# Kernel tuning notes

Measured on AMD Instinct MI355X. Metric: run time of the kernel, lower is better.

The kernel has to match this reference:

```python
import jax, jax.numpy as jnp
import numpy as np

D_MODEL = 512
NHEAD = 8
WINDOW = 64


def setup_inputs() -> dict:
    key = jax.random.key(0)
    ks = jax.random.split(key, 5)
    d = D_MODEL
    x = jax.random.normal(ks[0], (8, 2048, d), dtype=jnp.float32)
    # nn.MultiheadAttention params: packed in-proj [3d, d] + bias [3d], out-proj [d, d] + bias [d]
    scale = 1.0 / np.sqrt(d)
    in_proj_w = jax.random.normal(ks[1], (3 * d, d), dtype=jnp.float32) * scale
    in_proj_b = jnp.zeros((3 * d,), dtype=jnp.float32)
    out_proj_w = jax.random.normal(ks[2], (d, d), dtype=jnp.float32) * scale
    out_proj_b = jnp.zeros((d,), dtype=jnp.float32)
    return {"x": x, "in_proj_w": in_proj_w, "in_proj_b": in_proj_b,
            "out_proj_w": out_proj_w, "out_proj_b": out_proj_b}


def reference(x, in_proj_w, in_proj_b, out_proj_w, out_proj_b):
    B, L, d = x.shape
    H = NHEAD
    dh = d // H
    # packed qkv projection (torch Linear: x @ W.T + b)
    qkv = jnp.einsum('bld,ed->ble', x, in_proj_w) + in_proj_b  # [B, L, 3d]
    q, k, v = jnp.split(qkv, 3, axis=-1)
    # split heads -> [B, H, L, dh]
    def heads(t):
        return t.reshape(B, L, H, dh).transpose(0, 2, 1, 3)
    q, k, v = heads(q), heads(k), heads(v)
    scores = jnp.einsum('bhqd,bhkd->bhqk', q, k) / jnp.sqrt(jnp.float32(dh))
    # banded mask: positions with |i-j| > window are masked out
    idx = jnp.arange(L)
    band = jnp.abs(idx[None, :] - idx[:, None]) > WINDOW  # [L, L] bool
    scores = jnp.where(band[None, None, :, :], jnp.float32(-jnp.inf), scores)
    p = jax.nn.softmax(scores, axis=-1)
    out = jnp.einsum('bhqk,bhkd->bhqd', p, v)  # [B, H, L, dh]
    out = out.transpose(0, 2, 1, 3).reshape(B, L, d)
    return jnp.einsum('bld,ed->ble', out, out_proj_w) + out_proj_b
```

## Files before the change

kernel.cpp:

```cpp
#include <hip/hip_runtime.h>

typedef __bf16 bf16x8 __attribute__((ext_vector_type(8)));
typedef unsigned short u16;
typedef unsigned short u16x8 __attribute__((ext_vector_type(8)));
typedef float f32x4 __attribute__((ext_vector_type(4)));

#define L_SEQ 2048
#define NQT   (L_SEQ / 128)
#define SB()  __builtin_amdgcn_sched_barrier(0)

__device__ __forceinline__ float bf2f(u16 x) {
    unsigned u = ((unsigned)x) << 16;
    return __builtin_bit_cast(float, u);
}
__device__ __forceinline__ u16 f2bf(float f) {
    unsigned u = __builtin_bit_cast(unsigned, f);
    u += 0x7FFFu + ((u >> 16) & 1u);
    return (u16)(u >> 16);
}

__device__ __forceinline__ void gload_lds16(const u16* g, u16* l) {
    __builtin_amdgcn_global_load_lds(
        (const __attribute__((address_space(1))) void*)g,
        (__attribute__((address_space(3))) void*)l, 16, 0, 0);
}

__global__ void cvt_w(const float* __restrict__ wi, const float* __restrict__ wo,
                      u16* __restrict__ wio, u16* __restrict__ woo,
                      int nwi8, int nwo8) {
    int i = blockIdx.x * blockDim.x + threadIdx.x;
    const float* src; u16* dst;
    if (i < nwi8) { src = wi; dst = wio; }
    else if (i < nwi8 + nwo8) { i -= nwi8; src = wo; dst = woo; }
    else return;
    const float4* p = reinterpret_cast<const float4*>(src) + (size_t)i * 2;
    const float4 a = p[0], b = p[1];
    u16x8 r;
    r[0] = f2bf(a.x); r[1] = f2bf(a.y); r[2] = f2bf(a.z); r[3] = f2bf(a.w);
    r[4] = f2bf(b.x); r[5] = f2bf(b.y); r[6] = f2bf(b.z); r[7] = f2bf(b.w);
    *(reinterpret_cast<u16x8*>(dst) + i) = r;
}

__launch_bounds__(512, 4)
__global__ void gemm_qkv(const float* __restrict__ A, const u16* __restrict__ W,
                         const float* __restrict__ bias, u16* __restrict__ C,
                         int M, int N, int K) {
    __shared__ u16 As[3][256 * 32];
    __shared__ u16 Bs[3][128 * 32];

    const int tid   = threadIdx.x;
    const int lane  = tid & 63;
    const int wid   = tid >> 6;
    const int wm    = wid >> 1;
    const int wn    = wid & 1;
    const int row_l = lane & 15;
    const int grp   = lane >> 4;

    const int nwg  = gridDim.x * gridDim.y;
    const int hw   = blockIdx.y * gridDim.x + blockIdx.x;
    const int tile = (hw & 7) * (nwg >> 3) + (hw >> 3);
    const int m0 = (tile / gridDim.x) * 256;
    const int n0 = (tile % gridDim.x) * 128;

    const int arow = tid >> 1;
    const int av   = (arow >> 1) & 3;
    const int g0   = ((tid & 1) * 2)     ^ av;
    const int g1   = ((tid & 1) * 2 + 1) ^ av;
    const float* gA0 = A + (size_t)(m0 + arow) * K + g0 * 8;
    const float* gA1 = A + (size_t)(m0 + arow) * K + g1 * 8;

    const int brow = tid >> 2;
    const int bcol = ((tid & 3) ^ ((tid >> 3) & 3)) * 8;
    const u16* gB = W + (size_t)(n0 + brow) * K + bcol;

    f32x4 acc[4][4];
#pragma unroll
    for (int mi = 0; mi < 4; ++mi)
#pragma unroll
        for (int ni = 0; ni < 4; ++ni)
            acc[mi][ni] = (f32x4){0.f, 0.f, 0.f, 0.f};

    const int rchunk = (grp ^ ((row_l >> 1) & 3)) * 8;
    const int NT = K >> 5;

    {
        const f32x4* q0 = reinterpret_cast<const f32x4*>(gA0);
        const f32x4* q1 = reinterpret_cast<const f32x4*>(gA1);
        f32x4 p00 = q0[0], p01 = q0[1], p10 = q1[0], p11 = q1[1];
        SB();
        gload_lds16(gB,      &Bs[0][0] + wid * 512);
        SB();
        gload_lds16(gB + 32, &Bs[1][0] + wid * 512);
        SB();
        asm volatile("s_waitcnt vmcnt(2)" ::: "memory");
        SB();
        u16x8 w0, w1;
#pragma unroll
        for (int e = 0; e < 4; ++e) {
            w0[e] = f2bf(p00[e]); w0[4 + e] = f2bf(p01[e]);
            w1[e] = f2bf(p10[e]); w1[4 + e] = f2bf(p11[e]);
        }
        *reinterpret_cast<u16x8*>(&As[0][(2 * tid + 0) * 8]) = w0;
        *reinterpret_cast<u16x8*>(&As[0][(2 * tid + 1) * 8]) = w1;
        asm volatile("s_waitcnt vmcnt(1)" ::: "memory");
        asm volatile("s_waitcnt lgkmcnt(0)" ::: "memory");
        __builtin_amdgcn_s_barrier();
    }

    int buf = 0;
    for (int t = 0; t < NT; ++t) {
        bf16x8 a[4], b[4];
#pragma unroll
        for (int mi = 0; mi < 4; ++mi)
            a[mi] = *reinterpret_cast<const bf16x8*>(
                &As[buf][(wm * 64 + mi * 16 + row_l) * 32 + rchunk]);
#pragma unroll
        for (int ni = 0; ni < 4; ++ni)
            b[ni] = *reinterpret_cast<const bf16x8*>(
                &Bs[buf][(wn * 64 + ni * 16 + row_l) * 32 + rchunk]);
        SB();
        f32x4 p00, p01, p10, p11;
        if (t + 1 < NT) {
            const f32x4* q0 = reinterpret_cast<const f32x4*>(gA0 + (t + 1) * 32);
            const f32x4* q1 = reinterpret_cast<const f32x4*>(gA1 + (t + 1) * 32);
            p00 = q0[0]; p01 = q0[1]; p10 = q1[0]; p11 = q1[1];
        }
        SB();
        if (t + 2 < NT) {
            int sb = buf + 2; if (sb >= 3) sb -= 3;
            gload_lds16(gB + (size_t)(t + 2) * 32, &Bs[sb][0] + wid * 512);
        }
        SB();
        asm volatile("s_waitcnt lgkmcnt(0)" ::: "memory");
        SB();
        __builtin_amdgcn_s_setprio(1);
#pragma unroll
        for (int mi = 0; mi < 4; ++mi)
#pragma unroll
            for (int ni = 0; ni < 4; ++ni)
                acc[mi][ni] = __builtin_amdgcn_mfma_f32_16x16x32_bf16(a[mi], b[ni], acc[mi][ni], 0, 0, 0);
        __builtin_amdgcn_s_setprio(0);
        SB();
        if (t + 1 < NT) {
            if (t + 2 < NT) asm volatile("s_waitcnt vmcnt(1)" ::: "memory");
            else            asm volatile("s_waitcnt vmcnt(0)" ::: "memory");
            SB();
            int wb = buf + 1; if (wb >= 3) wb -= 3;
            u16x8 w0, w1;
#pragma unroll
            for (int e = 0; e < 4; ++e) {
                w0[e] = f2bf(p00[e]); w0[4 + e] = f2bf(p01[e]);
                w1[e] = f2bf(p10[e]); w1[4 + e] = f2bf(p11[e]);
            }
            *reinterpret_cast<u16x8*>(&As[wb][(2 * tid + 0) * 8]) = w0;
            *reinterpret_cast<u16x8*>(&As[wb][(2 * tid + 1) * 8]) = w1;
            asm volatile("s_waitcnt lgkmcnt(0)" ::: "memory");
            __builtin_amdgcn_s_barrier();
        }
        buf = buf + 1; if (buf >= 3) buf = 0;
    }

#pragma unroll
    for (int ni = 0; ni < 4; ++ni) {
        const int col = n0 + wn * 64 + ni * 16 + row_l;
        const float bsf = bias[col];
#pragma unroll
        for (int mi = 0; mi < 4; ++mi) {
#pragma unroll
            for (int r = 0; r < 4; ++r) {
                const int rowm = m0 + wm * 64 + mi * 16 + grp * 4 + r;
                C[(size_t)rowm * N + col] = f2bf(acc[mi][ni][r] + bsf);
            }
        }
    }
}

template <bool OUT_BF16>
__launch_bounds__(256, 3)
__global__ void gemm_ring(const u16* __restrict__ A, const u16* __restrict__ W,
                          const float* __restrict__ bias, void* __restrict__ Cv,
                          int M, int N, int K) {
    __shared__ u16 As[3][128 * 32];
    __shared__ u16 Bs[3][128 * 32];

    const int tid   = threadIdx.x;
    const int lane  = tid & 63;
    const int wid   = tid >> 6;
    const int wm    = wid >> 1;
    const int wn    = wid & 1;
    const int row_l = lane & 15;
    const int grp   = lane >> 4;

    const int nwg  = gridDim.x * gridDim.y;
    const int hw   = blockIdx.y * gridDim.x + blockIdx.x;
    const int tile = (hw & 7) * (nwg >> 3) + (hw >> 3);
    const int m0 = (tile / gridDim.x) * 128;
    const int n0 = (tile % gridDim.x) * 128;

    const int srow = tid >> 2;
    const int scol = ((tid & 3) ^ ((tid >> 3) & 3)) * 8;
    const u16* gA = A + (size_t)(m0 + srow) * K + scol;
    const u16* gB = W + (size_t)(n0 + srow) * K + scol;

    f32x4 acc[4][4];
#pragma unroll
    for (int mi = 0; mi < 4; ++mi)
#pragma unroll
        for (int ni = 0; ni < 4; ++ni)
            acc[mi][ni] = (f32x4){0.f, 0.f, 0.f, 0.f};

    auto stage = [&](int buf, int kt) {
#pragma unroll
        for (int i = 0; i < 2; ++i) {
            gload_lds16(gA + (size_t)(i * 64) * K + kt * 32, &As[buf][i * 2048 + wid * 512]);
            gload_lds16(gB + (size_t)(i * 64) * K + kt * 32, &Bs[buf][i * 2048 + wid * 512]);
        }
    };

    const int rchunk = (grp ^ ((row_l >> 1) & 3)) * 8;

    auto compute = [&](int buf) {
        bf16x8 a[4], b[4];
#pragma unroll
        for (int mi = 0; mi < 4; ++mi)
            a[mi] = *reinterpret_cast<const bf16x8*>(
                &As[buf][(wm * 64 + mi * 16 + row_l) * 32 + rchunk]);
#pragma unroll
        for (int ni = 0; ni < 4; ++ni)
            b[ni] = *reinterpret_cast<const bf16x8*>(
                &Bs[buf][(wn * 64 + ni * 16 + row_l) * 32 + rchunk]);
        __builtin_amdgcn_s_setprio(1);
#pragma unroll
        for (int mi = 0; mi < 4; ++mi)
#pragma unroll
            for (int ni = 0; ni < 4; ++ni)
                acc[mi][ni] = __builtin_amdgcn_mfma_f32_16x16x32_bf16(a[mi], b[ni], acc[mi][ni], 0, 0, 0);
        __builtin_amdgcn_s_setprio(0);
    };

    const int NT = K >> 5;
    stage(0, 0);
    stage(1, 1);
    int cur = 0;
    for (int t = 0; t < NT; ++t) {
        if (t == NT - 1) asm volatile("s_waitcnt vmcnt(0)" ::: "memory");
        else             asm volatile("s_waitcnt vmcnt(4)" ::: "memory");
        __builtin_amdgcn_s_barrier();
        if (t + 2 < NT) {
            int st = cur + 2; if (st >= 3) st -= 3;
            stage(st, t + 2);
        }
        compute(cur);
        cur = cur + 1; if (cur >= 3) cur = 0;
    }

#pragma unroll
    for (int ni = 0; ni < 4; ++ni) {
        const int col = n0 + wn * 64 + ni * 16 + row_l;
        const float bsf = bias[col];
#pragma unroll
        for (int mi = 0; mi < 4; ++mi) {
#pragma unroll
            for (int r = 0; r < 4; ++r) {
                const int rowm = m0 + wm * 64 + mi * 16 + grp * 4 + r;
                const float v = acc[mi][ni][r] + bsf;
                if (OUT_BF16)
                    ((u16*)Cv)[(size_t)rowm * N + col] = f2bf(v);
                else
                    ((float*)Cv)[(size_t)rowm * N + col] = v;
            }
        }
    }
}

__launch_bounds__(512, 4)
__global__ void local_attn(const u16* __restrict__ qkv, u16* __restrict__ att) {
    __shared__ __align__(16) u16 Ks[256 * 64];
    __shared__ __align__(16) u16 Vt[64 * 256];
    __shared__ __align__(16) u16 Pl[8][512];

    const int tid   = threadIdx.x;
    const int lane  = tid & 63;
    const int wv    = tid >> 6;
    const int row_l = lane & 15;
    const int grp   = lane >> 4;
    const int qt = blockIdx.x, h = blockIdx.y, b = blockIdx.z;
    const int q0b = qt * 128;
    const int kstart = q0b - 64;
    const size_t base = (size_t)b * L_SEQ * 1536;
    const bool edge = (qt == 0) || (qt == NQT - 1);

    {
        const int r0 = tid >> 3;
        const int c  = tid & 7;
#pragma unroll
        for (int i = 0; i < 4; ++i) {
            const int row  = i * 64 + r0;
            const int keyg = min(max(kstart + row, 0), L_SEQ - 1);
            const int cg   = c ^ (row & 7);
            gload_lds16(qkv + base + (size_t)keyg * 1536 + 512 + h * 64 + cg * 8,
                        &Ks[i * 4096 + wv * 512]);
        }
    }
    {
#pragma unroll
        for (int i = 0; i < 4; ++i) {
            const int idx  = i * 512 + tid;
            const int row  = idx >> 3;
            const int c8   = idx & 7;
            const int keyg = min(max(kstart + row, 0), L_SEQ - 1);
            const u16x8 vu = *reinterpret_cast<const u16x8*>(
                qkv + base + (size_t)keyg * 1536 + 1024 + h * 64 + c8 * 8);
#pragma unroll
            for (int e = 0; e < 8; ++e) {
                const int d = c8 * 8 + e;
                const int slot = (row >> 3) ^ (d & 7) ^ ((d >> 3) & 7);
                Vt[d * 256 + slot * 8 + (row & 7)] = vu[e];
            }
        }
    }

    const int qrow_g = q0b + wv * 16 + row_l;
    const u16* qp = qkv + base + (size_t)qrow_g * 1536 + h * 64;
    const bf16x8 qf0 = *reinterpret_cast<const bf16x8*>(qp + grp * 8);
    const bf16x8 qf1 = *reinterpret_cast<const bf16x8*>(qp + 32 + grp * 8);

    __syncthreads();

    float m_r = -1e30f, l_r = 0.f;
    f32x4 acc[4];
#pragma unroll
    for (int ds = 0; ds < 4; ++ds) acc[ds] = (f32x4){0.f, 0.f, 0.f, 0.f};
    u16* Pw = Pl[wv];

    auto do_chunk = [&](int c, bool bandLo, bool bandHi, bool half, bool rng) {
        const int kcL = wv * 16 + 32 * c;
        const int kcG = kstart + kcL;
        const int nf = half ? 1 : 2;

        f32x4 s[2];
#pragma unroll
        for (int f = 0; f < 2; ++f) {
            if (f >= nf) break;
            const int rr = kcL + 16 * f + row_l;
            const bf16x8 ka = *reinterpret_cast<const bf16x8*>(
                &Ks[rr * 64 + ((grp ^ (rr & 7)) * 8)]);
            const bf16x8 kb = *reinterpret_cast<const bf16x8*>(
                &Ks[rr * 64 + (((grp + 4) ^ (rr & 7)) * 8)]);
            f32x4 z = (f32x4){0.f, 0.f, 0.f, 0.f};
            z = __builtin_amdgcn_mfma_f32_16x16x32_bf16(ka, qf0, z, 0, 0, 0);
            z = __builtin_amdgcn_mfma_f32_16x16x32_bf16(kb, qf1, z, 0, 0, 0);
            s[f] = z;
        }

        float p[2][4];
        float cmax = -1e30f;
#pragma unroll
        for (int f = 0; f < 2; ++f) {
            if (f >= nf) break;
#pragma unroll
            for (int r = 0; r < 4; ++r) {
                const int k = 16 * f + grp * 4 + r;
                bool ok = true;
                if (bandLo) ok = ok && (k >= row_l);
                if (bandHi) ok = ok && (k <= row_l);
                if (rng) { const int kg = kcG + k; ok = ok && (kg >= 0) && (kg < L_SEQ); }
                const float sv = ok ? s[f][r] * 0.125f : -1e30f;
                p[f][r] = sv;
                cmax = fmaxf(cmax, sv);
            }
        }
        cmax = fmaxf(cmax, __shfl_xor(cmax, 16, 64));
        cmax = fmaxf(cmax, __shfl_xor(cmax, 32, 64));

        const bool need = !__all(cmax <= m_r + 8.f);
        float mu;
        float scl = 1.f;
        if (need) {
            const float mn = fmaxf(m_r, cmax);
            scl = __expf(m_r - mn);
            m_r = mn;
            mu  = mn;
        } else {
            mu = m_r;
        }

        float lsum = 0.f;
#pragma unroll
        for (int f = 0; f < 2; ++f) {
            if (f >= nf) break;
#pragma unroll
            for (int r = 0; r < 4; ++r) {
                const float pv = (p[f][r] <= -1e29f) ? 0.f : __expf(p[f][r] - mu);
                p[f][r] = pv;
                lsum += pv;
            }
        }
        lsum += __shfl_xor(lsum, 16, 64);
        lsum += __shfl_xor(lsum, 32, 64);
        l_r = l_r * scl + lsum;

        if (need) {
            float scl4[4];
#pragma unroll
            for (int r = 0; r < 4; ++r) scl4[r] = __shfl(scl, grp * 4 + r, 64);
#pragma unroll
            for (int ds = 0; ds < 4; ++ds)
#pragma unroll
                for (int r = 0; r < 4; ++r) acc[ds][r] *= scl4[r];
        }

#pragma unroll
        for (int f = 0; f < 2; ++f)
#pragma unroll
            for (int r = 0; r < 4; ++r) {
                const int k = 16 * f + grp * 4 + r;
                const int slot = (k >> 3) ^ ((row_l >> 1) & 3);
                const float pv = (f < nf) ? p[f][r] : 0.f;
                Pw[row_l * 32 + slot * 8 + (k & 7)] = f2bf(pv);
            }
        const bf16x8 pa = *reinterpret_cast<const bf16x8*>(
            &Pw[row_l * 32 + ((grp ^ ((row_l >> 1) & 3)) * 8)]);

        int k0 = kcL + grp * 8;
        if (half) k0 = min(k0, 248);
#pragma unroll
        for (int ds = 0; ds < 4; ++ds) {
            const int d = ds * 16 + row_l;
            const int slot = (k0 >> 3) ^ (d & 7) ^ ((d >> 3) & 7);
            const bf16x8 vf = *reinterpret_cast<const bf16x8*>(
                &Vt[d * 256 + slot * 8]);
            acc[ds] = __builtin_amdgcn_mfma_f32_16x16x32_bf16(pa, vf, acc[ds], 0, 0, 0);
        }
    };

    if (!edge) {
        do_chunk(0, true,  false, false, false);
        do_chunk(1, false, false, false, false);
        do_chunk(2, false, false, false, false);
        do_chunk(3, false, false, false, false);
        do_chunk(4, false, true,  true,  false);
    } else {
        const int kw = kstart + wv * 16;
        if (kw       > -32 && kw       < L_SEQ) do_chunk(0, true,  false, false, true);
        if (kw + 32  > -32 && kw + 32  < L_SEQ) do_chunk(1, false, false, false, true);
        if (kw + 64  > -32 && kw + 64  < L_SEQ) do_chunk(2, false, false, false, true);
        if (kw + 96  > -32 && kw + 96  < L_SEQ) do_chunk(3, false, false, false, true);
        if (kw + 128 > -32 && kw + 128 < L_SEQ) do_chunk(4, false, true,  true,  true);
    }

    const float inv = 1.f / l_r;
    float inv4[4];
#pragma unroll
    for (int r = 0; r < 4; ++r) inv4[r] = __shfl(inv, grp * 4 + r, 64);
    const int qg = q0b + wv * 16 + grp * 4;
#pragma unroll
    for (int r = 0; r < 4; ++r)
#pragma unroll
        for (int ds = 0; ds < 4; ++ds)
            att[(size_t)(b * L_SEQ + qg + r) * 512 + h * 64 + ds * 16 + row_l] =
                f2bf(acc[ds][r] * inv4[r]);
}

extern "C" void kernel_launch(void* const* d_in, const int* in_sizes, int n_in,
                              void* d_out, int out_size, void* d_ws, size_t ws_size,
                              hipStream_t stream) {
    const float* x     = (const float*)d_in[0];
    const float* w_in  = (const float*)d_in[1];
    const float* b_in  = (const float*)d_in[2];
    const float* w_out = (const float*)d_in[3];
    const float* b_out = (const float*)d_in[4];
    float* out = (float*)d_out;

    const int B = 8, L = L_SEQ;
    const int M = B * L;

    u16* qkv   = (u16*)d_ws;
    u16* att   = qkv   + (size_t)M * 1536;
    u16* wi_bf = att   + (size_t)M * 512;
    u16* wo_bf = wi_bf + (size_t)1536 * 512;

    const int nwi8 = 1536 * 512 / 8;
    const int nwo8 = 512 * 512 / 8;
    const int ncvt = nwi8 + nwo8;
    cvt_w<<<(ncvt + 255) / 256, 256, 0, stream>>>(w_in, w_out, wi_bf, wo_bf, nwi8, nwo8);

    gemm_qkv<<<dim3(1536 / 128, M / 256), dim3(512), 0, stream>>>(
        x, wi_bf, b_in, qkv, M, 1536, 512);

    local_attn<<<dim3(NQT, 8, B), dim3(512), 0, stream>>>(qkv, att);

    gemm_ring<false><<<dim3(512 / 128, M / 128), dim3(256), 0, stream>>>(
        att, wo_bf, b_out, out, M, 512, 512);
}
```

Before: 102.3 us.

## Deepen QKV GEMM A-prefetch pipeline and enlarge output GEMM tiles to 256x128

The QKV GEMM now prefetches the fp32 activation tile two k-steps ahead. It converts and writes the next bf16 A tile into LDS before the MFMA block instead of after it, so global loads overlap more compute. The A load mapping changes to row-per-quad chunks with an XOR swizzle. The output projection GEMM becomes a 512-thread kernel with 256x128 tiles and a three-buffer LDS ring with explicit waitcnts and barriers. This halves the number of workgroups, at the cost of more registers held in flight and tighter synchronisation.

```diff
diff --git a/kernel.cpp b/kernel.cpp
--- a/kernel.cpp
+++ b/kernel.cpp
@@ -42,7 +42,7 @@
 }
 
 __launch_bounds__(512, 4)
-__global__ void gemm_qkv(const float* __restrict__ A, const u16* __restrict__ W,
+__global__ void gemm_qkv(const float* __restrict__ X, const u16* __restrict__ W,
                          const float* __restrict__ bias, u16* __restrict__ C,
                          int M, int N, int K) {
     __shared__ u16 As[3][256 * 32];
@@ -62,12 +62,11 @@
     const int m0 = (tile / gridDim.x) * 256;
     const int n0 = (tile % gridDim.x) * 128;
 
-    const int arow = tid >> 1;
-    const int av   = (arow >> 1) & 3;
-    const int g0   = ((tid & 1) * 2)     ^ av;
-    const int g1   = ((tid & 1) * 2 + 1) ^ av;
-    const float* gA0 = A + (size_t)(m0 + arow) * K + g0 * 8;
-    const float* gA1 = A + (size_t)(m0 + arow) * K + g1 * 8;
+    const int ag  = (tid & 3) ^ ((tid >> 3) & 3);
+    const float* gX0 = X + (size_t)(m0 + (tid >> 2)) * K + ag * 8;
+    const float* gX1 = gX0 + (size_t)128 * K;
+    u16* wA0 = &As[0][0] + tid * 8;
+    u16* wA1 = &As[0][0] + (512 + tid) * 8;
 
     const int brow = tid >> 2;
     const int bcol = ((tid & 3) ^ ((tid >> 3) & 3)) * 8;
@@ -83,29 +82,39 @@
     const int rchunk = (grp ^ ((row_l >> 1) & 3)) * 8;
     const int NT = K >> 5;
 
-    {
-        const f32x4* q0 = reinterpret_cast<const f32x4*>(gA0);
-        const f32x4* q1 = reinterpret_cast<const f32x4*>(gA1);
-        f32x4 p00 = q0[0], p01 = q0[1], p10 = q1[0], p11 = q1[1];
-        SB();
-        gload_lds16(gB,      &Bs[0][0] + wid * 512);
-        SB();
-        gload_lds16(gB + 32, &Bs[1][0] + wid * 512);
-        SB();
-        asm volatile("s_waitcnt vmcnt(2)" ::: "memory");
-        SB();
+    f32x4 pa0, pa1, pa2, pa3;
+
+    auto issueA = [&](int kt) {
+        const f32x4* q0 = reinterpret_cast<const f32x4*>(gX0 + kt * 32);
+        const f32x4* q1 = reinterpret_cast<const f32x4*>(gX1 + kt * 32);
+        pa0 = q0[0]; pa1 = q0[1]; pa2 = q1[0]; pa3 = q1[1];
+    };
+    auto writeA = [&](int buf) {
         u16x8 w0, w1;
 #pragma unroll
         for (int e = 0; e < 4; ++e) {
-            w0[e] = f2bf(p00[e]); w0[4 + e] = f2bf(p01[e]);
-            w1[e] = f2bf(p10[e]); w1[4 + e] = f2bf(p11[e]);
-        }
-        *reinterpret_cast<u16x8*>(&As[0][(2 * tid + 0) * 8]) = w0;
-        *reinterpret_cast<u16x8*>(&As[0][(2 * tid + 1) * 8]) = w1;
-        asm volatile("s_waitcnt vmcnt(1)" ::: "memory");
-        asm volatile("s_waitcnt lgkmcnt(0)" ::: "memory");
-        __builtin_amdgcn_s_barrier();
-    }
+            w0[e] = f2bf(pa0[e]); w0[4 + e] = f2bf(pa1[e]);
+            w1[e] = f2bf(pa2[e]); w1[4 + e] = f2bf(pa3[e]);
+        }
+        *reinterpret_cast<u16x8*>(wA0 + buf * 8192) = w0;
+        *reinterpret_cast<u16x8*>(wA1 + buf * 8192) = w1;
+    };
+
+    issueA(0);
+    SB();
+    gload_lds16(gB, &Bs[0][0] + wid * 512);
+    SB();
+    asm volatile("s_waitcnt vmcnt(1)" ::: "memory");
+    SB();
+    writeA(0);
+    SB();
+    issueA(1);
+    SB();
+    gload_lds16(gB + 32, &Bs[1][0] + wid * 512);
+    SB();
+    asm volatile("s_waitcnt vmcnt(5)" ::: "memory");
+    asm volatile("s_waitcnt lgkmcnt(0)" ::: "memory");
+    __builtin_amdgcn_s_barrier();
 
     int buf = 0;
     for (int t = 0; t < NT; ++t) {
@@ -118,21 +127,31 @@
         for (int ni = 0; ni < 4; ++ni)
             b[ni] = *reinterpret_cast<const bf16x8*>(
                 &Bs[buf][(wn * 64 + ni * 16 + row_l) * 32 + rchunk]);
-        SB();
-        f32x4 p00, p01, p10, p11;
-        if (t + 1 < NT) {
-            const f32x4* q0 = reinterpret_cast<const f32x4*>(gA0 + (t + 1) * 32);
-            const f32x4* q1 = reinterpret_cast<const f32x4*>(gA1 + (t + 1) * 32);
-            p00 = q0[0]; p01 = q0[1]; p10 = q1[0]; p11 = q1[1];
-        }
-        SB();
-        if (t + 2 < NT) {
-            int sb = buf + 2; if (sb >= 3) sb -= 3;
-            gload_lds16(gB + (size_t)(t + 2) * 32, &Bs[sb][0] + wid * 512);
-        }
-        SB();
         asm volatile("s_waitcnt lgkmcnt(0)" ::: "memory");
         SB();
+
+        const int nxt = (buf + 1 < 3) ? buf + 1 : buf - 2;
+        const int n2  = (buf + 2 < 3) ? buf + 2 : buf - 1;
+
+        if (t + 1 < NT) {
+            asm volatile("s_waitcnt vmcnt(1)" ::: "memory");
+            SB();
+            writeA(nxt);
+            SB();
+        }
+        if (t + 2 < NT) {
+            issueA(t + 2);
+            SB();
+            gload_lds16(gB + (size_t)(t + 2) * 32, &Bs[n2][0] + wid * 512);
+            SB();
+            asm volatile("s_waitcnt vmcnt(5)" ::: "memory");
+        } else {
+            asm volatile("s_waitcnt vmcnt(0)" ::: "memory");
+        }
+        asm volatile("s_waitcnt lgkmcnt(0)" ::: "memory");
+        if (t + 1 < NT) __builtin_amdgcn_s_barrier();
+        SB();
+
         __builtin_amdgcn_s_setprio(1);
 #pragma unroll
         for (int mi = 0; mi < 4; ++mi)
@@ -140,24 +159,7 @@
             for (int ni = 0; ni < 4; ++ni)
                 acc[mi][ni] = __builtin_amdgcn_mfma_f32_16x16x32_bf16(a[mi], b[ni], acc[mi][ni], 0, 0, 0);
         __builtin_amdgcn_s_setprio(0);
-        SB();
-        if (t + 1 < NT) {
-            if (t + 2 < NT) asm volatile("s_waitcnt vmcnt(1)" ::: "memory");
-            else            asm volatile("s_waitcnt vmcnt(0)" ::: "memory");
-            SB();
-            int wb = buf + 1; if (wb >= 3) wb -= 3;
-            u16x8 w0, w1;
-#pragma unroll
-            for (int e = 0; e < 4; ++e) {
-                w0[e] = f2bf(p00[e]); w0[4 + e] = f2bf(p01[e]);
-                w1[e] = f2bf(p10[e]); w1[4 + e] = f2bf(p11[e]);
-            }
-            *reinterpret_cast<u16x8*>(&As[wb][(2 * tid + 0) * 8]) = w0;
-            *reinterpret_cast<u16x8*>(&As[wb][(2 * tid + 1) * 8]) = w1;
-            asm volatile("s_waitcnt lgkmcnt(0)" ::: "memory");
-            __builtin_amdgcn_s_barrier();
-        }
-        buf = buf + 1; if (buf >= 3) buf = 0;
+        buf = nxt;
     }
 
 #pragma unroll
@@ -175,12 +177,11 @@
     }
 }
 
-template <bool OUT_BF16>
-__launch_bounds__(256, 3)
-__global__ void gemm_ring(const u16* __restrict__ A, const u16* __restrict__ W,
-                          const float* __restrict__ bias, void* __restrict__ Cv,
-                          int M, int N, int K) {
-    __shared__ u16 As[3][128 * 32];
+__launch_bounds__(512, 4)
+__global__ void gemm_out(const u16* __restrict__ A, const u16* __restrict__ W,
+                         const float* __restrict__ bias, float* __restrict__ Cv,
+                         int M, int N, int K) {
+    __shared__ u16 As[3][256 * 32];
     __shared__ u16 Bs[3][128 * 32];
 
     const int tid   = threadIdx.x;
@@ -194,7 +195,7 @@
     const int nwg  = gridDim.x * gridDim.y;
     const int hw   = blockIdx.y * gridDim.x + blockIdx.x;
     const int tile = (hw & 7) * (nwg >> 3) + (hw >> 3);
-    const int m0 = (tile / gridDim.x) * 128;
+    const int m0 = (tile / gridDim.x) * 256;
     const int n0 = (tile % gridDim.x) * 128;
 
     const int srow = tid >> 2;
@@ -209,17 +210,22 @@
         for (int ni = 0; ni < 4; ++ni)
             acc[mi][ni] = (f32x4){0.f, 0.f, 0.f, 0.f};
 
-    auto stage = [&](int buf, int kt) {
-#pragma unroll
-        for (int i = 0; i < 2; ++i) {
-            gload_lds16(gA + (size_t)(i * 64) * K + kt * 32, &As[buf][i * 2048 + wid * 512]);
-            gload_lds16(gB + (size_t)(i * 64) * K + kt * 32, &Bs[buf][i * 2048 + wid * 512]);
-        }
+    auto stage = [&](int b2, int kt) {
+        gload_lds16(gA + (size_t)kt * 32,                   &As[b2][0]    + wid * 512);
+        gload_lds16(gA + (size_t)128 * K + (size_t)kt * 32, &As[b2][4096] + wid * 512);
+        gload_lds16(gB + (size_t)kt * 32,                   &Bs[b2][0]    + wid * 512);
     };
 
     const int rchunk = (grp ^ ((row_l >> 1) & 3)) * 8;
 
-    auto compute = [&](int buf) {
+    const int NT = K >> 5;
+    stage(0, 0);
+    stage(1, 1);
+    asm volatile("s_waitcnt vmcnt(3)" ::: "memory");
+    __builtin_amdgcn_s_barrier();
+
+    int buf = 0;
+    for (int kt = 0; kt < NT; ++kt) {
         bf16x8 a[4], b[4];
 #pragma unroll
         for (int mi = 0; mi < 4; ++mi)
@@ -229,6 +235,16 @@
         for (int ni = 0; ni < 4; ++ni)
             b[ni] = *reinterpret_cast<const bf16x8*>(
                 &Bs[buf][(wn * 64 + ni * 16 + row_l) * 32 + rchunk]);
+
+        if (kt + 2 < NT) {
+            int st = buf + 2; if (st >= 3) st -= 3;
+            stage(st, kt + 2);
+        }
+        if (kt < NT - 2)       asm volatile("s_waitcnt vmcnt(3)" ::: "memory");
+        else if (kt == NT - 2) asm volatile("s_waitcnt vmcnt(0)" ::: "memory");
+        __builtin_amdgcn_s_barrier();
+        asm volatile("s_waitcnt lgkmcnt(0)" ::: "memory");
+        __builtin_amdgcn_sched_barrier(0);
         __builtin_amdgcn_s_setprio(1);
 #pragma unroll
         for (int mi = 0; mi < 4; ++mi)
@@ -236,22 +252,8 @@
             for (int ni = 0; ni < 4; ++ni)
                 acc[mi][ni] = __builtin_amdgcn_mfma_f32_16x16x32_bf16(a[mi], b[ni], acc[mi][ni], 0, 0, 0);
         __builtin_amdgcn_s_setprio(0);
-    };
-
-    const int NT = K >> 5;
-    stage(0, 0);
-    stage(1, 1);
-    int cur = 0;
-    for (int t = 0; t < NT; ++t) {
-        if (t == NT - 1) asm volatile("s_waitcnt vmcnt(0)" ::: "memory");
-        else             asm volatile("s_waitcnt vmcnt(4)" ::: "memory");
         __builtin_amdgcn_s_barrier();
-        if (t + 2 < NT) {
-            int st = cur + 2; if (st >= 3) st -= 3;
-            stage(st, t + 2);
-        }
-        compute(cur);
-        cur = cur + 1; if (cur >= 3) cur = 0;
+        buf = buf + 1; if (buf >= 3) buf = 0;
     }
 
 #pragma unroll
@@ -263,11 +265,7 @@
 #pragma unroll
             for (int r = 0; r < 4; ++r) {
                 const int rowm = m0 + wm * 64 + mi * 16 + grp * 4 + r;
-                const float v = acc[mi][ni][r] + bsf;
-                if (OUT_BF16)
-                    ((u16*)Cv)[(size_t)rowm * N + col] = f2bf(v);
-                else
-                    ((float*)Cv)[(size_t)rowm * N + col] = v;
+                Cv[(size_t)rowm * N + col] = acc[mi][ni][r] + bsf;
             }
         }
     }
@@ -490,6 +488,6 @@
 
     local_attn<<<dim3(NQT, 8, B), dim3(512), 0, stream>>>(qkv, att);
 
-    gemm_ring<false><<<dim3(512 / 128, M / 128), dim3(256), 0, stream>>>(
+    gemm_out<<<dim3(512 / 128, M / 256), dim3(512), 0, stream>>>(
         att, wo_bf, b_out, out, M, 512, 512);
 }
```

Measured after the change: 158.4 us. +54.8%, slower.
